# Kernel optimization log

Measured on AMD Instinct MI355X. Metric: run time of the kernel, lower is better.

## Reference

```python
import jax, jax.numpy as jnp
import numpy as np

E, N, H, F = 8, 16384, 1024, 4096  # experts, total tokens, hidden, ffn hidden

def setup_inputs() -> dict:
    key = jax.random.key(0)
    k1, k2, k3 = jax.random.split(key, 3)
    x = jax.random.normal(k1, (N, H), dtype=jnp.float32)
    # original uses torch.rand for weights -> uniform [0,1)
    w1 = jax.random.uniform(k2, (E, H, F), dtype=jnp.float32)
    w2 = jax.random.uniform(k3, (E, F, H), dtype=jnp.float32)
    tokens_per_expert = jnp.full((E,), N // E, dtype=jnp.int32)
    return {
        "permuted_local_hidden_states": x,
        "weight1": w1,
        "weight2": w2,
        "tokens_per_expert": tokens_per_expert,
    }

def reference(permuted_local_hidden_states, weight1, weight2, tokens_per_expert):
    # Grouped GEMM 1: per-expert x[rows_e] @ w1[e]  -> [N, F]
    fc1_output = jax.lax.ragged_dot(permuted_local_hidden_states, weight1, tokens_per_expert)
    # Unfused activation (F.gelu default = exact erf gelu)
    intermediate = jax.nn.gelu(fc1_output, approximate=False)
    # Grouped GEMM 2: per-expert act[rows_e] @ w2[e] -> [N, H]
    fc2_output = jax.lax.ragged_dot(intermediate, weight2, tokens_per_expert)
    return fc2_output
```

## Files before the change

kernel.cpp:

```cpp
#include <hip/hip_runtime.h>
#include <hip/hip_bf16.h>

typedef unsigned short u16;
typedef __attribute__((ext_vector_type(8))) __bf16 bf16x8;
typedef __attribute__((ext_vector_type(4))) float f32x4;
typedef __attribute__((ext_vector_type(4))) float f4v;
typedef __attribute__((ext_vector_type(8))) unsigned short u16x8;

__device__ __forceinline__ u16 f32_to_bf16(float f) {
  unsigned int u = __builtin_bit_cast(unsigned int, f);
  u += 0x7FFFu + ((u >> 16) & 1u);
  return (u16)(u >> 16);
}

__device__ __forceinline__ float fast_gelu(float v) {
  float v2 = v * v;
  float t = v * fmaf(0.0713548162726f, v2, 1.5957691216057308f);
  float e = __expf(-t);
  float s = __builtin_amdgcn_rcpf(1.0f + e);
  return v * s;
}

__device__ __forceinline__ void async_ld16(const void* gsrc, void* ldst) {
  __builtin_amdgcn_global_load_lds(
      (__attribute__((address_space(1))) void*)(unsigned long long)gsrc,
      (__attribute__((address_space(3))) void*)(unsigned long long)ldst,
      16, 0, 0);
}

__global__ void cvt_kernel(const float* __restrict__ in, u16* __restrict__ out, int n8) {
  int i = blockIdx.x * blockDim.x + threadIdx.x;
  if (i >= n8) return;
  const f4v* p = (const f4v*)(in + (size_t)i * 8);
  f4v a = p[0], b = p[1];
  u16x8 r;
  r[0] = f32_to_bf16(a[0]); r[1] = f32_to_bf16(a[1]);
  r[2] = f32_to_bf16(a[2]); r[3] = f32_to_bf16(a[3]);
  r[4] = f32_to_bf16(b[0]); r[5] = f32_to_bf16(b[1]);
  r[6] = f32_to_bf16(b[2]); r[7] = f32_to_bf16(b[3]);
  *(u16x8*)(out + (size_t)i * 8) = r;
}

__global__ void tpose_cvt_kernel(const float* __restrict__ in, u16* __restrict__ out,
                                 int R, int C) {
  __shared__ u16 tile[32][33];
  const int e = blockIdx.z;
  const int c0 = blockIdx.x * 32, r0 = blockIdx.y * 32;
  const float* src = in + (size_t)e * R * C;
  u16* dst = out + (size_t)e * R * C;
  const int tx = threadIdx.x, ty = threadIdx.y;
#pragma unroll
  for (int i = 0; i < 32; i += 8)
    tile[ty + i][tx] = f32_to_bf16(src[(size_t)(r0 + ty + i) * C + (c0 + tx)]);
  __syncthreads();
#pragma unroll
  for (int i = 0; i < 32; i += 8)
    dst[(size_t)(c0 + ty + i) * R + (r0 + tx)] = tile[tx][ty + i];
}

template <int FUSE>
__global__ __launch_bounds__(256)
void grouped_gemm(const u16* __restrict__ A, const u16* __restrict__ Bt,
                  void* __restrict__ Out, const int* __restrict__ tokens,
                  int Mtot, int K, int Nn) {
  const int NT = Nn >> 7;
  const int id = blockIdx.x;
  const int xcd = id & 7;
  const int within = id >> 3;
  const int slot = xcd + 8 * (within / NT);
  const int ntile = within % NT;

  int row_start = 0, tiles_before = 0;
  int expert = -1, my_row0 = 0, rows_valid = 0;
#pragma unroll
  for (int e = 0; e < 8; ++e) {
    int t = tokens[e];
    int nt = (t + 127) >> 7;
    if (expert < 0 && slot >= tiles_before && slot < tiles_before + nt) {
      expert = e;
      int mi = slot - tiles_before;
      my_row0 = row_start + mi * 128;
      rows_valid = t - mi * 128;
      if (rows_valid > 128) rows_valid = 128;
    }
    tiles_before += nt;
    row_start += t;
  }
  if (expert < 0) return;

  const int n0 = ntile * 128;
  const u16* Bq = Bt + (size_t)expert * Nn * K + (size_t)n0 * K;

  __shared__ __align__(16) u16 lA[2][128 * 32];
  __shared__ __align__(16) u16 lB[2][128 * 32];

  const int tid = threadIdx.x;
  const int lane = tid & 63;
  const int wave = tid >> 6;
  const int wm = (wave >> 1) * 64;
  const int wn = (wave & 1) * 64;
  const int fr = lane & 15;
  const int fq = lane >> 4;

  f32x4 acc[4][4];
#pragma unroll
  for (int i = 0; i < 4; ++i)
#pragma unroll
    for (int j = 0; j < 4; ++j) acc[i][j] = (f32x4){0.f, 0.f, 0.f, 0.f};

  const int sr = tid >> 2;
  const int swz = ((tid & 3) ^ ((sr >> 1) & 3)) * 8;
  int ga0 = my_row0 + sr;       if (ga0 > Mtot - 1) ga0 = Mtot - 1;
  int ga1 = my_row0 + 64 + sr;  if (ga1 > Mtot - 1) ga1 = Mtot - 1;
  const u16* pA0 = A + (size_t)ga0 * K + swz;
  const u16* pA1 = A + (size_t)ga1 * K + swz;
  const u16* pB0 = Bq + (size_t)sr * K + swz;
  const u16* pB1 = Bq + (size_t)(64 + sr) * K + swz;

  const int cswz = (fq ^ ((fr >> 1) & 3)) * 8;

  async_ld16(pA0, &lA[0][tid * 8]);
  async_ld16(pA1, &lA[0][2048 + tid * 8]);
  async_ld16(pB0, &lB[0][tid * 8]);
  async_ld16(pB1, &lB[0][2048 + tid * 8]);

  int buf = 0;
  for (int k0 = 0; k0 < K; k0 += 32) {
    __syncthreads();
    if (k0 + 32 < K) {
      const int nb = buf ^ 1;
      async_ld16(pA0 + k0 + 32, &lA[nb][tid * 8]);
      async_ld16(pA1 + k0 + 32, &lA[nb][2048 + tid * 8]);
      async_ld16(pB0 + k0 + 32, &lB[nb][tid * 8]);
      async_ld16(pB1 + k0 + 32, &lB[nb][2048 + tid * 8]);
    }

    bf16x8 aF[4], bF[4];
#pragma unroll
    for (int i = 0; i < 4; ++i)
      aF[i] = *(const bf16x8*)&lA[buf][(wm + i * 16 + fr) * 32 + cswz];
#pragma unroll
    for (int j = 0; j < 4; ++j)
      bF[j] = *(const bf16x8*)&lB[buf][(wn + j * 16 + fr) * 32 + cswz];
#pragma unroll
    for (int i = 0; i < 4; ++i)
#pragma unroll
      for (int j = 0; j < 4; ++j)
        acc[i][j] = __builtin_amdgcn_mfma_f32_16x16x32_bf16(aF[i], bF[j], acc[i][j], 0, 0, 0);
    buf ^= 1;
  }

  if (FUSE) {
    u16* Op = (u16*)Out;
#pragma unroll
    for (int i = 0; i < 4; ++i) {
#pragma unroll
      for (int r = 0; r < 4; ++r) {
        int lrow = wm + i * 16 + fq * 4 + r;
        if (lrow < rows_valid) {
          size_t base = (size_t)(my_row0 + lrow) * Nn + (size_t)(n0 + wn + fr);
#pragma unroll
          for (int j = 0; j < 4; ++j)
            Op[base + j * 16] = f32_to_bf16(fast_gelu(acc[i][j][r]));
        }
      }
    }
  } else {
    float* Op = (float*)Out;
#pragma unroll
    for (int i = 0; i < 4; ++i) {
#pragma unroll
      for (int r = 0; r < 4; ++r) {
        int lrow = wm + i * 16 + fq * 4 + r;
        if (lrow < rows_valid) {
          size_t base = (size_t)(my_row0 + lrow) * Nn + (size_t)(n0 + wn + fr);
#pragma unroll
          for (int j = 0; j < 4; ++j) Op[base + j * 16] = acc[i][j][r];
        }
      }
    }
  }
}

extern "C" void kernel_launch(void* const* d_in, const int* in_sizes, int n_in,
                              void* d_out, int out_size, void* d_ws, size_t ws_size,
                              hipStream_t stream) {
  (void)in_sizes; (void)n_in; (void)out_size; (void)ws_size;
  const float* x  = (const float*)d_in[0];
  const float* w1 = (const float*)d_in[1];
  const float* w2 = (const float*)d_in[2];
  const int* tokens = (const int*)d_in[3];

  const int N = 16384, H = 1024, F = 4096, E = 8;

  u16* x_bf  = (u16*)d_ws;
  u16* w1t   = x_bf + (size_t)N * H;
  u16* w2t   = w1t + (size_t)E * F * H;
  u16* inter = w2t + (size_t)E * H * F;

  cvt_kernel<<<dim3((N * H / 8 + 255) / 256), dim3(256), 0, stream>>>(x, x_bf, N * H / 8);
  tpose_cvt_kernel<<<dim3(F / 32, H / 32, E), dim3(32, 8), 0, stream>>>(w1, w1t, H, F);
  tpose_cvt_kernel<<<dim3(H / 32, F / 32, E), dim3(32, 8), 0, stream>>>(w2, w2t, F, H);

  const int SLOTS = N / 128 + E;
  grouped_gemm<1><<<dim3((F / 128) * SLOTS), dim3(256), 0, stream>>>(
      x_bf, w1t, inter, tokens, N, H, F);
  grouped_gemm<0><<<dim3((H / 128) * SLOTS), dim3(256), 0, stream>>>(
      inter, w2t, (float*)d_out, tokens, N, F, H);
}
```

Baseline: 721.0 us.

## Enlarge GEMM tiles to 256x256 with 4-stage async pipeline and vectorized transpose

The grouped GEMM moves from 128x128 tiles with 256 threads to 256x256 tiles with 512 threads and 8 waves. Each wave computes a 128x64 block. It uses a 4-buffer LDS ring with a 3-slice prefetch depth, split barriers, and s_setprio around the MFMA bursts to overlap loads with math and raise operand reuse. The weight transpose/convert kernel is rewritten to use 64x64 tiles with float4 loads and 4-element packed stores. The larger tiles raise LDS use (64KB) and register pressure, and they leave fewer blocks for the second GEMM.

After: 631.9 us. -12.4%, faster.

```diff
diff --git a/kernel.cpp b/kernel.cpp
--- a/kernel.cpp
+++ b/kernel.cpp
@@ -5,6 +5,8 @@
 typedef __attribute__((ext_vector_type(8))) __bf16 bf16x8;
 typedef __attribute__((ext_vector_type(4))) float f32x4;
 typedef __attribute__((ext_vector_type(4))) float f4v;
+typedef __attribute__((ext_vector_type(2))) unsigned short u16x2;
+typedef __attribute__((ext_vector_type(4))) unsigned short u16x4;
 typedef __attribute__((ext_vector_type(8))) unsigned short u16x8;
 
 __device__ __forceinline__ u16 f32_to_bf16(float f) {
@@ -41,29 +43,43 @@
   *(u16x8*)(out + (size_t)i * 8) = r;
 }
 
-__global__ void tpose_cvt_kernel(const float* __restrict__ in, u16* __restrict__ out,
-                                 int R, int C) {
-  __shared__ u16 tile[32][33];
+__global__ __launch_bounds__(256)
+void tpose_cvt_kernel(const float* __restrict__ in, u16* __restrict__ out, int R, int C) {
+  __shared__ u16 tile[64 * 66];
   const int e = blockIdx.z;
-  const int c0 = blockIdx.x * 32, r0 = blockIdx.y * 32;
+  const int c0 = blockIdx.x * 64, r0 = blockIdx.y * 64;
   const float* src = in + (size_t)e * R * C;
   u16* dst = out + (size_t)e * R * C;
-  const int tx = threadIdx.x, ty = threadIdx.y;
-#pragma unroll
-  for (int i = 0; i < 32; i += 8)
-    tile[ty + i][tx] = f32_to_bf16(src[(size_t)(r0 + ty + i) * C + (c0 + tx)]);
+  const int t = threadIdx.x;
+#pragma unroll
+  for (int i = 0; i < 4; ++i) {
+    int idx = i * 256 + t;
+    int row = idx >> 4, c4 = idx & 15;
+    f4v v = *(const f4v*)&src[(size_t)(r0 + row) * C + (c0 + c4 * 4)];
+    u16x2 lo, hi;
+    lo[0] = f32_to_bf16(v[0]); lo[1] = f32_to_bf16(v[1]);
+    hi[0] = f32_to_bf16(v[2]); hi[1] = f32_to_bf16(v[3]);
+    *(u16x2*)&tile[row * 66 + c4 * 4] = lo;
+    *(u16x2*)&tile[row * 66 + c4 * 4 + 2] = hi;
+  }
   __syncthreads();
 #pragma unroll
-  for (int i = 0; i < 32; i += 8)
-    dst[(size_t)(c0 + ty + i) * R + (r0 + tx)] = tile[tx][ty + i];
+  for (int i = 0; i < 4; ++i) {
+    int idx = i * 256 + t;
+    int c = idx >> 4, r4 = idx & 15;
+    u16x4 v;
+#pragma unroll
+    for (int j = 0; j < 4; ++j) v[j] = tile[(r4 * 4 + j) * 66 + c];
+    *(u16x4*)&dst[(size_t)(c0 + c) * R + r0 + r4 * 4] = v;
+  }
 }
 
 template <int FUSE>
-__global__ __launch_bounds__(256)
+__global__ __launch_bounds__(512, 2)
 void grouped_gemm(const u16* __restrict__ A, const u16* __restrict__ Bt,
                   void* __restrict__ Out, const int* __restrict__ tokens,
                   int Mtot, int K, int Nn) {
-  const int NT = Nn >> 7;
+  const int NT = Nn >> 8;
   const int id = blockIdx.x;
   const int xcd = id & 7;
   const int within = id >> 3;
@@ -74,108 +90,128 @@
   int expert = -1, my_row0 = 0, rows_valid = 0;
 #pragma unroll
   for (int e = 0; e < 8; ++e) {
-    int t = tokens[e];
-    int nt = (t + 127) >> 7;
+    int tk = tokens[e];
+    int nt = (tk + 255) >> 8;
     if (expert < 0 && slot >= tiles_before && slot < tiles_before + nt) {
       expert = e;
       int mi = slot - tiles_before;
-      my_row0 = row_start + mi * 128;
-      rows_valid = t - mi * 128;
-      if (rows_valid > 128) rows_valid = 128;
+      my_row0 = row_start + mi * 256;
+      rows_valid = tk - mi * 256;
+      if (rows_valid > 256) rows_valid = 256;
     }
     tiles_before += nt;
-    row_start += t;
+    row_start += tk;
   }
   if (expert < 0) return;
 
-  const int n0 = ntile * 128;
+  const int n0 = ntile * 256;
   const u16* Bq = Bt + (size_t)expert * Nn * K + (size_t)n0 * K;
 
-  __shared__ __align__(16) u16 lA[2][128 * 32];
-  __shared__ __align__(16) u16 lB[2][128 * 32];
+  __shared__ __align__(16) u16 lA[4][8192];
+  __shared__ __align__(16) u16 lB[4][8192];
 
   const int tid = threadIdx.x;
   const int lane = tid & 63;
   const int wave = tid >> 6;
-  const int wm = (wave >> 1) * 64;
-  const int wn = (wave & 1) * 64;
+  const int wm = (wave >> 2) * 128;
+  const int wn = (wave & 3) * 64;
   const int fr = lane & 15;
   const int fq = lane >> 4;
 
-  f32x4 acc[4][4];
-#pragma unroll
-  for (int i = 0; i < 4; ++i)
+  f32x4 acc[8][4];
+#pragma unroll
+  for (int i = 0; i < 8; ++i)
 #pragma unroll
     for (int j = 0; j < 4; ++j) acc[i][j] = (f32x4){0.f, 0.f, 0.f, 0.f};
 
   const int sr = tid >> 2;
   const int swz = ((tid & 3) ^ ((sr >> 1) & 3)) * 8;
-  int ga0 = my_row0 + sr;       if (ga0 > Mtot - 1) ga0 = Mtot - 1;
-  int ga1 = my_row0 + 64 + sr;  if (ga1 > Mtot - 1) ga1 = Mtot - 1;
+  int ga0 = my_row0 + sr;        if (ga0 > Mtot - 1) ga0 = Mtot - 1;
+  int ga1 = my_row0 + 128 + sr;  if (ga1 > Mtot - 1) ga1 = Mtot - 1;
   const u16* pA0 = A + (size_t)ga0 * K + swz;
   const u16* pA1 = A + (size_t)ga1 * K + swz;
   const u16* pB0 = Bq + (size_t)sr * K + swz;
-  const u16* pB1 = Bq + (size_t)(64 + sr) * K + swz;
+  const u16* pB1 = Bq + (size_t)(128 + sr) * K + swz;
 
   const int cswz = (fq ^ ((fr >> 1) & 3)) * 8;
-
-  async_ld16(pA0, &lA[0][tid * 8]);
-  async_ld16(pA1, &lA[0][2048 + tid * 8]);
-  async_ld16(pB0, &lB[0][tid * 8]);
-  async_ld16(pB1, &lB[0][2048 + tid * 8]);
-
-  int buf = 0;
-  for (int k0 = 0; k0 < K; k0 += 32) {
-    __syncthreads();
-    if (k0 + 32 < K) {
-      const int nb = buf ^ 1;
-      async_ld16(pA0 + k0 + 32, &lA[nb][tid * 8]);
-      async_ld16(pA1 + k0 + 32, &lA[nb][2048 + tid * 8]);
-      async_ld16(pB0 + k0 + 32, &lB[nb][tid * 8]);
-      async_ld16(pB1 + k0 + 32, &lB[nb][2048 + tid * 8]);
-    }
-
-    bf16x8 aF[4], bF[4];
-#pragma unroll
-    for (int i = 0; i < 4; ++i)
-      aF[i] = *(const bf16x8*)&lA[buf][(wm + i * 16 + fr) * 32 + cswz];
-#pragma unroll
-    for (int j = 0; j < 4; ++j)
-      bF[j] = *(const bf16x8*)&lB[buf][(wn + j * 16 + fr) * 32 + cswz];
-#pragma unroll
-    for (int i = 0; i < 4; ++i)
-#pragma unroll
-      for (int j = 0; j < 4; ++j)
-        acc[i][j] = __builtin_amdgcn_mfma_f32_16x16x32_bf16(aF[i], bF[j], acc[i][j], 0, 0, 0);
-    buf ^= 1;
+  const int aoff0 = (wm + fr) * 32 + cswz;
+  const int boff0 = (wn + fr) * 32 + cswz;
+
+  const int nslices = K >> 5;
+
+#pragma unroll
+  for (int s = 0; s < 3; ++s) {
+    async_ld16(pA0 + s * 32, &lA[s][tid * 8]);
+    async_ld16(pA1 + s * 32, &lA[s][4096 + tid * 8]);
+    async_ld16(pB0 + s * 32, &lB[s][tid * 8]);
+    async_ld16(pB1 + s * 32, &lB[s][4096 + tid * 8]);
+  }
+
+  bf16x8 aF[4], bF[4];
+  for (int sl = 0; sl < nslices; ++sl) {
+    const int b = sl & 3;
+    const int nb = (sl + 3) & 3;
+    const int sk = (sl + 3 < nslices ? sl + 3 : sl) * 32;
+
+    asm volatile("s_waitcnt vmcnt(8)" ::: "memory");
+    __builtin_amdgcn_s_barrier();
+    asm volatile("" ::: "memory");
+
+    async_ld16(pA0 + sk, &lA[nb][tid * 8]);
+    async_ld16(pA1 + sk, &lA[nb][4096 + tid * 8]);
+#pragma unroll
+    for (int n = 0; n < 4; ++n) bF[n] = *(const bf16x8*)&lB[b][boff0 + n * 512];
+#pragma unroll
+    for (int m = 0; m < 4; ++m) aF[m] = *(const bf16x8*)&lA[b][aoff0 + m * 512];
+    __builtin_amdgcn_s_setprio(1);
+#pragma unroll
+    for (int m = 0; m < 4; ++m)
+#pragma unroll
+      for (int n = 0; n < 4; ++n)
+        acc[m][n] = __builtin_amdgcn_mfma_f32_16x16x32_bf16(aF[m], bF[n], acc[m][n], 0, 0, 0);
+    __builtin_amdgcn_s_setprio(0);
+    __builtin_amdgcn_s_barrier();
+    asm volatile("" ::: "memory");
+
+    async_ld16(pB0 + sk, &lB[nb][tid * 8]);
+    async_ld16(pB1 + sk, &lB[nb][4096 + tid * 8]);
+#pragma unroll
+    for (int m = 0; m < 4; ++m) aF[m] = *(const bf16x8*)&lA[b][aoff0 + 2048 + m * 512];
+    __builtin_amdgcn_s_setprio(1);
+#pragma unroll
+    for (int m = 0; m < 4; ++m)
+#pragma unroll
+      for (int n = 0; n < 4; ++n)
+        acc[m + 4][n] = __builtin_amdgcn_mfma_f32_16x16x32_bf16(aF[m], bF[n], acc[m + 4][n], 0, 0, 0);
+    __builtin_amdgcn_s_setprio(0);
   }
 
   if (FUSE) {
     u16* Op = (u16*)Out;
 #pragma unroll
-    for (int i = 0; i < 4; ++i) {
+    for (int m = 0; m < 8; ++m) {
 #pragma unroll
       for (int r = 0; r < 4; ++r) {
-        int lrow = wm + i * 16 + fq * 4 + r;
+        int lrow = wm + m * 16 + fq * 4 + r;
         if (lrow < rows_valid) {
           size_t base = (size_t)(my_row0 + lrow) * Nn + (size_t)(n0 + wn + fr);
 #pragma unroll
-          for (int j = 0; j < 4; ++j)
-            Op[base + j * 16] = f32_to_bf16(fast_gelu(acc[i][j][r]));
+          for (int n = 0; n < 4; ++n)
+            Op[base + n * 16] = f32_to_bf16(fast_gelu(acc[m][n][r]));
         }
       }
     }
   } else {
     float* Op = (float*)Out;
 #pragma unroll
-    for (int i = 0; i < 4; ++i) {
+    for (int m = 0; m < 8; ++m) {
 #pragma unroll
       for (int r = 0; r < 4; ++r) {
-        int lrow = wm + i * 16 + fq * 4 + r;
+        int lrow = wm + m * 16 + fq * 4 + r;
         if (lrow < rows_valid) {
           size_t base = (size_t)(my_row0 + lrow) * Nn + (size_t)(n0 + wn + fr);
 #pragma unroll
-          for (int j = 0; j < 4; ++j) Op[base + j * 16] = acc[i][j][r];
+          for (int n = 0; n < 4; ++n) Op[base + n * 16] = acc[m][n][r];
         }
       }
     }
@@ -199,12 +235,12 @@
   u16* inter = w2t + (size_t)E * H * F;
 
   cvt_kernel<<<dim3((N * H / 8 + 255) / 256), dim3(256), 0, stream>>>(x, x_bf, N * H / 8);
-  tpose_cvt_kernel<<<dim3(F / 32, H / 32, E), dim3(32, 8), 0, stream>>>(w1, w1t, H, F);
-  tpose_cvt_kernel<<<dim3(H / 32, F / 32, E), dim3(32, 8), 0, stream>>>(w2, w2t, F, H);
-
-  const int SLOTS = N / 128 + E;
-  grouped_gemm<1><<<dim3((F / 128) * SLOTS), dim3(256), 0, stream>>>(
+  tpose_cvt_kernel<<<dim3(F / 64, H / 64, E), dim3(256), 0, stream>>>(w1, w1t, H, F);
+  tpose_cvt_kernel<<<dim3(H / 64, F / 64, E), dim3(256), 0, stream>>>(w2, w2t, F, H);
+
+  const int SLOTS = N / 256 + E;
+  grouped_gemm<1><<<dim3((F / 256) * SLOTS), dim3(512), 0, stream>>>(
       x_bf, w1t, inter, tokens, N, H, F);
-  grouped_gemm<0><<<dim3((H / 128) * SLOTS), dim3(256), 0, stream>>>(
+  grouped_gemm<0><<<dim3((H / 256) * SLOTS), dim3(512), 0, stream>>>(
       inter, w2t, (float*)d_out, tokens, N, F, H);
 }
```
